# Performance work log

Measured on AMD Instinct MI355X. Metric: run time of the kernel, lower is better.

The kernel has to match this reference:

```python
import jax, jax.numpy as jnp
import numpy as np

N, E = 50000, 800000
IN, HID, OUT = 128, 256, 40
EPS = 1e-5


def setup_inputs() -> dict:
    key = jax.random.key(0)
    ks = jax.random.split(key, 16)
    def glorot(k, shape):
        lim = float(np.sqrt(6.0 / (shape[0] + shape[1])))
        return jax.random.uniform(k, shape, jnp.float32, -lim, lim)
    return {
        "x": jax.random.normal(ks[0], (N, IN), jnp.float32),
        "edge_index": jax.random.randint(ks[1], (2, E), 0, N, jnp.int64),
        "W1": glorot(ks[2], (IN, HID)),  "b1": jnp.zeros((HID,), jnp.float32),
        "g1": jnp.ones((HID,), jnp.float32), "be1": jnp.zeros((HID,), jnp.float32),
        "W2": glorot(ks[3], (HID, HID)), "b2": jnp.zeros((HID,), jnp.float32),
        "g2": jnp.ones((HID,), jnp.float32), "be2": jnp.zeros((HID,), jnp.float32),
        "W3": glorot(ks[4], (HID, OUT)), "b3": jnp.zeros((OUT,), jnp.float32),
        "Wl": glorot(ks[5], (OUT, OUT)), "bl": jnp.zeros((OUT,), jnp.float32),
    }


def _gcn_conv(h, src, dst, norm, W, b, n):
    # PyG GCNConv: transform, then normalized scatter-add over edges (+self-loops)
    m = h @ W                                     # [N, d_out]
    msg = m[src] * norm[:, None]                  # gather + edge scale
    out = jax.ops.segment_sum(msg, dst, num_segments=n)
    return out + b


def _bn(h, g, b):
    # BatchNorm1d (training-mode batch stats, biased variance)
    mu = jnp.mean(h, axis=0)
    var = jnp.var(h, axis=0)
    return (h - mu) * jax.lax.rsqrt(var + EPS) * g + b


def reference(x, edge_index, W1, b1, g1, be1, W2, b2, g2, be2, W3, b3, Wl, bl):
    n = x.shape[0]
    loops = jnp.arange(n, dtype=edge_index.dtype)
    src = jnp.concatenate([edge_index[0], loops])
    dst = jnp.concatenate([edge_index[1], loops])
    deg = jax.ops.segment_sum(jnp.ones(src.shape[0], x.dtype), dst, num_segments=n)
    dinv = jnp.where(deg > 0, jax.lax.rsqrt(deg), 0.0)
    norm = dinv[src] * dinv[dst]

    h = jax.nn.relu(_bn(_gcn_conv(x, src, dst, norm, W1, b1, n), g1, be1))
    h = jax.nn.relu(_bn(_gcn_conv(h, src, dst, norm, W2, b2, n), g2, be2))
    h = _gcn_conv(h, src, dst, norm, W3, b3, n)
    h = h @ Wl + bl
    return jax.nn.log_softmax(h, axis=1)
```

## Files before the change

kernel.cpp:

```cpp
#include <hip/hip_runtime.h>
#include <hip/hip_bf16.h>
#include <math.h>

#define IN_DIM 128
#define HID 256
#define OUT_DIM 40
#define OUT_PAD 64
#define CAP 64
#define EPS 1e-5f

typedef __attribute__((ext_vector_type(8))) short short8;
typedef __attribute__((ext_vector_type(4))) float floatx4;

__device__ __forceinline__ float b2f(unsigned short u) {
    union { unsigned int i; float f; } c; c.i = ((unsigned int)u) << 16; return c.f;
}
__device__ __forceinline__ unsigned short f2b(float f) {
    union { float f; unsigned int i; } c; c.f = f;
    unsigned int r = c.i + 0x7FFF + ((c.i >> 16) & 1);
    return (unsigned short)(r >> 16);
}

union U8 { uint4 u; unsigned short s[8]; };
union F8 { short8 v; unsigned short s[8]; uint4 u; };


__global__ void fill1_k(const int* __restrict__ src, const int* __restrict__ dst,
                        int* __restrict__ cnt, int* __restrict__ col2, int E,
                        const float* __restrict__ W1, const float* __restrict__ W2,
                        const float* __restrict__ W3, const float* __restrict__ Wl,
                        const float* __restrict__ b3, const float* __restrict__ bl,
                        unsigned short* __restrict__ W1t, unsigned short* __restrict__ W2t,
                        unsigned short* __restrict__ W3lt, float* __restrict__ bias2,
                        float* __restrict__ stats1, float* __restrict__ stats2,
                        const float* __restrict__ x, unsigned short* __restrict__ xb,
                        int N) {
    if (blockIdx.x < 1024) {
        for (int e = blockIdx.x * 256 + threadIdx.x; e < E; e += 1024 * 256) {
            int d = dst[e];
            int p = atomicAdd(&cnt[d], 1);
            if (p < CAP) col2[d * CAP + p] = src[e];
        }
    } else if (blockIdx.x < 1536) {
        const int n1 = 256 * 128, n2 = 256 * 256;
        int j = (blockIdx.x - 1024) * 256 + threadIdx.x;
        if (j < n1) {
            int n = j >> 7, k = j & 127;
            W1t[j] = f2b(W1[k * 256 + n]);
        } else if (j < n1 + n2) {
            int j2 = j - n1;
            int n = j2 >> 8, k = j2 & 255;
            W2t[j2] = f2b(W2[k * 256 + n]);
        } else {
            int j3 = j - n1 - n2;
            int n = j3 >> 8, k = j3 & 255;
            float acc = 0.f;
            if (n < OUT_DIM) {
                for (int q = 0; q < OUT_DIM; ++q)
                    acc += W3[k * OUT_DIM + q] * Wl[q * OUT_DIM + n];
            }
            W3lt[j3] = (n < OUT_DIM) ? f2b(acc) : 0;
            if (j3 < OUT_DIM) {
                float b = bl[j3];
                for (int q = 0; q < OUT_DIM; ++q) b += b3[q] * Wl[q * OUT_DIM + j3];
                bias2[j3] = b;
            }
        }
    } else if (blockIdx.x == 1536) {
        int t = threadIdx.x;
        stats1[t] = 0.f; stats1[256 + t] = 0.f;
        stats2[t] = 0.f; stats2[256 + t] = 0.f;
    } else {
        size_t nx = (size_t)N * 32;
        size_t nbk = gridDim.x - 1537;
        for (size_t i = (size_t)(blockIdx.x - 1537) * 256 + threadIdx.x; i < nx;
             i += nbk * 256) {
            float4 v = ((const float4*)x)[i];
            ushort4 o;
            o.x = f2b(v.x); o.y = f2b(v.y); o.z = f2b(v.z); o.w = f2b(v.w);
            ((ushort4*)xb)[i] = o;
        }
    }
}


template <int MT, bool BN, bool STATS>
__global__ __launch_bounds__(64, 6) void gemm_w(const unsigned short* __restrict__ A,
                                                const unsigned short* __restrict__ Bt,
                                                unsigned short* __restrict__ C,
                                                const int* __restrict__ cnt,
                                                const float* __restrict__ bias,
                                                const float* __restrict__ bnstats,
                                                const float* __restrict__ g,
                                                const float* __restrict__ be,
                                                float* __restrict__ gstats,
                                                float invN,
                                                int M, int Nc, int K, int ldc) {
    __shared__ float s_sc[BN ? HID : 1], s_sh[BN ? HID : 1];
    int lane = threadIdx.x;
    if (BN) {
        for (int t = lane; t < K; t += 64) {
            float mu = bnstats[t] * invN;
            float var = bnstats[HID + t] * invN - mu * mu;
            float sc = g[t] * rsqrtf(var + EPS);
            s_sc[t] = sc;
            s_sh[t] = be[t] - mu * sc;
        }
        __syncthreads();
    }
    int r16 = lane & 15, quad = lane >> 4;
    int row0 = blockIdx.y * (MT * 16), col0 = blockIdx.x * 64;

    int arow[MT];
#pragma unroll
    for (int mt = 0; mt < MT; ++mt) arow[mt] = min(row0 + mt * 16 + r16, M - 1);

    floatx4 acc[MT][4] = {};

    for (int k0 = 0; k0 < K; k0 += 32) {
        int ka = k0 + quad * 8;
        F8 a[MT], b[4];
#pragma unroll
        for (int mt = 0; mt < MT; ++mt)
            a[mt].u = *(const uint4*)&A[(size_t)arow[mt] * K + ka];
#pragma unroll
        for (int nt = 0; nt < 4; ++nt)
            b[nt].u = *(const uint4*)&Bt[(size_t)(col0 + nt * 16 + r16) * K + ka];
        if (BN) {
            float4 sc0 = *(const float4*)&s_sc[ka];
            float4 sc1 = *(const float4*)&s_sc[ka + 4];
            float4 sh0 = *(const float4*)&s_sh[ka];
            float4 sh1 = *(const float4*)&s_sh[ka + 4];
            float sc[8] = {sc0.x, sc0.y, sc0.z, sc0.w, sc1.x, sc1.y, sc1.z, sc1.w};
            float sh[8] = {sh0.x, sh0.y, sh0.z, sh0.w, sh1.x, sh1.y, sh1.z, sh1.w};
#pragma unroll
            for (int mt = 0; mt < MT; ++mt)
#pragma unroll
                for (int j = 0; j < 8; ++j) {
                    float f = b2f(a[mt].s[j]) * sc[j] + sh[j];
                    a[mt].s[j] = f2b(fmaxf(f, 0.f));
                }
        }
#pragma unroll
        for (int mt = 0; mt < MT; ++mt)
#pragma unroll
            for (int nt = 0; nt < 4; ++nt)
                acc[mt][nt] = __builtin_amdgcn_mfma_f32_16x16x32_bf16(a[mt].v, b[nt].v, acc[mt][nt], 0, 0, 0);
    }

    float s1[4] = {0.f, 0.f, 0.f, 0.f}, s2[4] = {0.f, 0.f, 0.f, 0.f};
#pragma unroll
    for (int mt = 0; mt < MT; ++mt) {
#pragma unroll
        for (int r = 0; r < 4; ++r) {
            int row = row0 + mt * 16 + quad * 4 + r;
            if (row >= M) continue;
            float dv = cnt ? rsqrtf((float)(cnt[row] + 1)) : 1.f;
#pragma unroll
            for (int nt = 0; nt < 4; ++nt) {
                int colg = col0 + nt * 16 + r16;
                if (colg < Nc) {
                    float v = acc[mt][nt][r] * dv + (bias ? bias[colg] : 0.f);
                    C[(size_t)row * ldc + colg] = f2b(v);
                    if (STATS) { s1[nt] += v; s2[nt] += v * v; }
                }
            }
        }
    }
    if (STATS) {
#pragma unroll
        for (int nt = 0; nt < 4; ++nt) {
            s1[nt] += __shfl_xor(s1[nt], 16); s1[nt] += __shfl_xor(s1[nt], 32);
            s2[nt] += __shfl_xor(s2[nt], 16); s2[nt] += __shfl_xor(s2[nt], 32);
            if (quad == 0) {
                int colg = col0 + nt * 16 + r16;
                atomicAdd(&gstats[colg], s1[nt]);
                atomicAdd(&gstats[HID + colg], s2[nt]);
            }
        }
    }
}


__global__ __launch_bounds__(256, 8) void agg_x(const unsigned short* __restrict__ m,
                                                const int* __restrict__ col2,
                                                const int* __restrict__ cnt,
                                                unsigned short* __restrict__ out,
                                                int N) {
    int v = blockIdx.x * 4 + (threadIdx.x >> 6);
    if (v >= N) return;
    int lane = threadIdx.x & 63;
    int q = lane >> 4;
    int c0 = (lane & 15) * 8;
    int cv = cnt[v];
    float dv = rsqrtf((float)(cv + 1));
    const int* col = col2 + v * CAP;
    int end = min(cv, CAP);
    float a[8] = {};
    {
        U8 r; r.u = *(const uint4*)&m[(size_t)v * IN_DIM + c0];
#pragma unroll
        for (int k = 0; k < 8; ++k) a[k] = b2f(r.s[k]) * dv;
    }
    if (q != 0) { a[0]=a[1]=a[2]=a[3]=a[4]=a[5]=a[6]=a[7]=0.f; }
    int e = 0;
    for (; e + 8 <= end; e += 8) {
        int idx[2];
#pragma unroll
        for (int j = 0; j < 2; ++j) idx[j] = col[e + 4 * j + q];
        float ds[2];
#pragma unroll
        for (int j = 0; j < 2; ++j) ds[j] = rsqrtf((float)(cnt[idx[j]] + 1));
        U8 rr[2];
#pragma unroll
        for (int j = 0; j < 2; ++j)
            rr[j].u = *(const uint4*)&m[(size_t)idx[j] * IN_DIM + c0];
#pragma unroll
        for (int j = 0; j < 2; ++j)
#pragma unroll
            for (int k = 0; k < 8; ++k) a[k] += b2f(rr[j].s[k]) * ds[j];
    }
    for (; e < end; e += 4) {
        int t = e + q;
        if (t < end) {
            int s = col[t];
            float ds = rsqrtf((float)(cnt[s] + 1));
            U8 r; r.u = *(const uint4*)&m[(size_t)s * IN_DIM + c0];
#pragma unroll
            for (int k = 0; k < 8; ++k) a[k] += b2f(r.s[k]) * ds;
        }
    }
#pragma unroll
    for (int k = 0; k < 8; ++k) {
        a[k] += __shfl_xor(a[k], 16);
        a[k] += __shfl_xor(a[k], 32);
    }
    if (q == 0) {
        U8 o;
#pragma unroll
        for (int k = 0; k < 8; ++k) o.s[k] = f2b(a[k] * dv);
        *(uint4*)&out[(size_t)v * IN_DIM + c0] = o.u;
    }
}

__global__ __launch_bounds__(256, 8) void agg_h(const unsigned short* __restrict__ m,
                                                const int* __restrict__ col2,
                                                const int* __restrict__ cnt,
                                                const float* __restrict__ bias,
                                                unsigned short* __restrict__ out,
                                                int N) {
    int v = blockIdx.x * 4 + (threadIdx.x >> 6);
    if (v >= N) return;
    int lane = threadIdx.x & 63;
    int half = lane >> 5;
    int c0 = (lane & 31) * 8;
    int cv = cnt[v];
    float dv = rsqrtf((float)(cv + 1));
    const int* col = col2 + v * CAP;
    int end = min(cv, CAP);
    float a[8] = {};
    if (half == 0) {
        U8 r; r.u = *(const uint4*)&m[(size_t)v * HID + c0];
#pragma unroll
        for (int k = 0; k < 8; ++k) a[k] = b2f(r.s[k]);
    }
    int e = 0;
    for (; e + 8 <= end; e += 8) {
        int idx[4];
#pragma unroll
        for (int j = 0; j < 4; ++j) idx[j] = col[e + 2 * j + half];
        U8 rr[4];
#pragma unroll
        for (int j = 0; j < 4; ++j)
            rr[j].u = *(const uint4*)&m[(size_t)idx[j] * HID + c0];
#pragma unroll
        for (int j = 0; j < 4; ++j)
#pragma unroll
            for (int k = 0; k < 8; ++k) a[k] += b2f(rr[j].s[k]);
    }
    for (; e < end; e += 2) {
        int t = e + half;
        if (t < end) {
            U8 r; r.u = *(const uint4*)&m[(size_t)col[t] * HID + c0];
#pragma unroll
            for (int k = 0; k < 8; ++k) a[k] += b2f(r.s[k]);
        }
    }
#pragma unroll
    for (int k = 0; k < 8; ++k) a[k] += __shfl_xor(a[k], 32);
    if (half == 0) {
        U8 o;
#pragma unroll
        for (int k = 0; k < 8; ++k) o.s[k] = f2b(a[k] * dv + bias[c0 + k]);
        *(uint4*)&out[(size_t)v * HID + c0] = o.u;
    }
}

__global__ __launch_bounds__(256, 8) void agg_o_ls(const unsigned short* __restrict__ m,
                                                   const int* __restrict__ col2,
                                                   const int* __restrict__ cnt,
                                                   const float* __restrict__ bias2,
                                                   float* __restrict__ out,
                                                   int N) {
    int v = blockIdx.x * 4 + (threadIdx.x >> 6);
    if (v >= N) return;
    int lane = threadIdx.x & 63;
    int slot = lane >> 3;
    int li = lane & 7;
    int c0 = li * 8;
    int cv = cnt[v];
    float dv = rsqrtf((float)(cv + 1));
    const int* col = col2 + v * CAP;
    int end = min(cv, CAP);
    float a[8] = {};
    if (slot == 0) {
        U8 r; r.u = *(const uint4*)&m[(size_t)v * OUT_PAD + c0];
#pragma unroll
        for (int k = 0; k < 8; ++k) a[k] = b2f(r.s[k]);
    }
    int e = 0;
    for (; e + 16 <= end; e += 16) {
        int idx[2];
        idx[0] = col[e + slot];
        idx[1] = col[e + 8 + slot];
        U8 rr[2];
#pragma unroll
        for (int j = 0; j < 2; ++j)
            rr[j].u = *(const uint4*)&m[(size_t)idx[j] * OUT_PAD + c0];
#pragma unroll
        for (int j = 0; j < 2; ++j)
#pragma unroll
            for (int k = 0; k < 8; ++k) a[k] += b2f(rr[j].s[k]);
    }
    for (; e < end; e += 8) {
        int t = e + slot;
        if (t < end) {
            U8 r; r.u = *(const uint4*)&m[(size_t)col[t] * OUT_PAD + c0];
#pragma unroll
            for (int k = 0; k < 8; ++k) a[k] += b2f(r.s[k]);
        }
    }
#pragma unroll
    for (int k = 0; k < 8; ++k) {
        a[k] += __shfl_xor(a[k], 8);
        a[k] += __shfl_xor(a[k], 16);
        a[k] += __shfl_xor(a[k], 32);
    }
    bool valid = (li < 5);
    float mx = -INFINITY;
#pragma unroll
    for (int k = 0; k < 8; ++k) {
        float val = valid ? (a[k] * dv + bias2[c0 + k]) : -INFINITY;
        a[k] = val;
        mx = fmaxf(mx, val);
    }
    mx = fmaxf(mx, __shfl_xor(mx, 1));
    mx = fmaxf(mx, __shfl_xor(mx, 2));
    mx = fmaxf(mx, __shfl_xor(mx, 4));
    float s = 0.f;
    if (valid) {
#pragma unroll
        for (int k = 0; k < 8; ++k) s += expf(a[k] - mx);
    }
    s += __shfl_xor(s, 1);
    s += __shfl_xor(s, 2);
    s += __shfl_xor(s, 4);
    float ls = mx + logf(s);
    if (slot == 0 && valid) {
        float4 o0, o1;
        o0.x = a[0] - ls; o0.y = a[1] - ls; o0.z = a[2] - ls; o0.w = a[3] - ls;
        o1.x = a[4] - ls; o1.y = a[5] - ls; o1.z = a[6] - ls; o1.w = a[7] - ls;
        float* p = &out[(size_t)v * OUT_DIM + c0];
        *(float4*)p = o0;
        *(float4*)(p + 4) = o1;
    }
}


__global__ __launch_bounds__(256) void bn_stats(const unsigned short* __restrict__ h,
                                                float* __restrict__ stats, int N) {
    __shared__ float ls[8][2][256];
    int t = threadIdx.x;
    int walker = t >> 5;
    int c0 = (t & 31) * 8;
    int r0 = blockIdx.x * 128;
    int rend = min(r0 + 128, N);
    float s1[8] = {}, s2[8] = {};
    for (int r = r0 + walker; r < rend; r += 8) {
        U8 x; x.u = *(const uint4*)&h[(size_t)r * HID + c0];
#pragma unroll
        for (int k = 0; k < 8; ++k) {
            float v = b2f(x.s[k]);
            s1[k] += v; s2[k] += v * v;
        }
    }
#pragma unroll
    for (int k = 0; k < 8; ++k) {
        ls[walker][0][c0 + k] = s1[k];
        ls[walker][1][c0 + k] = s2[k];
    }
    __syncthreads();
    float a1 = 0.f, a2 = 0.f;
#pragma unroll
    for (int w = 0; w < 8; ++w) { a1 += ls[w][0][t]; a2 += ls[w][1][t]; }
    atomicAdd(&stats[t], a1);
    atomicAdd(&stats[HID + t], a2);
}


extern "C" void kernel_launch(void* const* d_in, const int* in_sizes, int n_in,
                              void* d_out, int out_size, void* d_ws, size_t ws_size,
                              hipStream_t stream) {
    const float* x   = (const float*)d_in[0];
    const int*  eidx = (const int*)d_in[1];
    const float* W1 = (const float*)d_in[2];
    const float* b1 = (const float*)d_in[3];
    const float* g1 = (const float*)d_in[4];
    const float* be1 = (const float*)d_in[5];
    const float* W2 = (const float*)d_in[6];
    const float* b2 = (const float*)d_in[7];
    const float* g2 = (const float*)d_in[8];
    const float* be2 = (const float*)d_in[9];
    const float* W3 = (const float*)d_in[10];
    const float* b3 = (const float*)d_in[11];
    const float* Wl = (const float*)d_in[12];
    const float* bl = (const float*)d_in[13];
    float* out = (float*)d_out;

    const int N = in_sizes[0] / IN_DIM;
    const int E = in_sizes[1] / 2;
    const int* src = eidx;
    const int* dst = eidx + E;

    size_t off = 0;
    char* ws = (char*)d_ws;
    auto carve = [&](size_t bytes) -> void* {
        void* p = ws + off;
        off += (bytes + 255) & ~(size_t)255;
        return p;
    };
    int*   cnt  = (int*)carve((size_t)N * 4);
    float* stats1 = (float*)carve((size_t)2 * HID * 4);
    float* stats2 = (float*)carve((size_t)2 * HID * 4);
    int*   col2 = (int*)carve((size_t)N * CAP * 4);
    unsigned short* xb   = (unsigned short*)carve((size_t)N * IN_DIM * 2);
    unsigned short* axb  = (unsigned short*)carve((size_t)N * IN_DIM * 2);
    unsigned short* W1t  = (unsigned short*)carve((size_t)256 * IN_DIM * 2);
    unsigned short* W2t  = (unsigned short*)carve((size_t)256 * HID * 2);
    unsigned short* W3lt = (unsigned short*)carve((size_t)128 * HID * 2);
    float* bias2 = (float*)carve((size_t)OUT_DIM * 4);
    unsigned short* mbuf = (unsigned short*)carve((size_t)N * HID * 2);
    unsigned short* hbuf = (unsigned short*)carve((size_t)N * HID * 2);

    hipMemsetAsync(cnt, 0, (size_t)N * 4, stream);
    int xconvBlocks = (int)(((size_t)N * 32 + 255) / 256);
    fill1_k<<<1537 + xconvBlocks, 256, 0, stream>>>(src, dst, cnt, col2, E,
                                                    W1, W2, W3, Wl, b3, bl,
                                                    W1t, W2t, W3lt, bias2,
                                                    stats1, stats2, x, xb, N);

    int nodeBlocks = (N + 3) / 4;
    float invN = 1.f / (float)N;
    int mb32 = (N + 31) / 32;
    int mb16 = (N + 15) / 16;

    agg_x<<<nodeBlocks, 256, 0, stream>>>(xb, col2, cnt, axb, N);
    gemm_w<2, false, true><<<dim3(4, mb32), 64, 0, stream>>>(axb, W1t, hbuf,
                                                             nullptr, b1,
                                                             nullptr, nullptr, nullptr,
                                                             stats1, invN,
                                                             N, HID, IN_DIM, HID);

    gemm_w<2, true, false><<<dim3(4, mb32), 64, 0, stream>>>(hbuf, W2t, mbuf,
                                                             cnt, nullptr,
                                                             stats1, g1, be1,
                                                             nullptr, invN,
                                                             N, HID, HID, HID);
    agg_h<<<nodeBlocks, 256, 0, stream>>>(mbuf, col2, cnt, b2, hbuf, N);
    bn_stats<<<(N + 127) / 128, 256, 0, stream>>>(hbuf, stats2, N);

    gemm_w<1, true, false><<<dim3(1, mb16), 64, 0, stream>>>(hbuf, W3lt, mbuf,
                                                             cnt, nullptr,
                                                             stats2, g2, be2,
                                                             nullptr, invN,
                                                             N, OUT_PAD, HID, OUT_PAD);
    agg_o_ls<<<nodeBlocks, 256, 0, stream>>>(mbuf, col2, cnt, bias2, out, N);
}
```

Baseline: 422.8 us.

## Stage GEMM tiles in LDS across multi-wave blocks and shrink CSR indices to 16-bit

Replaces the single-wave register-direct GEMM with a multi-wave kernel that stages A and B tiles through shared memory, so the B (weight) tile is loaded once per block and shared by 2-4 waves. BN stats are reduced in shared memory before the global atomics. The neighbor index buffer is stored as unsigned short, halving its footprint and gather traffic. The edge-fill phase also gets twice as many blocks. The 16-bit indices only hold for N ≤ 65536, so correctness depends on the input size. The new GEMM adds two block barriers per K step.

```diff
diff --git a/kernel.cpp b/kernel.cpp
--- a/kernel.cpp
+++ b/kernel.cpp
@@ -26,7 +26,7 @@
 
 
 __global__ void fill1_k(const int* __restrict__ src, const int* __restrict__ dst,
-                        int* __restrict__ cnt, int* __restrict__ col2, int E,
+                        int* __restrict__ cnt, unsigned short* __restrict__ col2, int E,
                         const float* __restrict__ W1, const float* __restrict__ W2,
                         const float* __restrict__ W3, const float* __restrict__ Wl,
                         const float* __restrict__ b3, const float* __restrict__ bl,
@@ -35,15 +35,15 @@
                         float* __restrict__ stats1, float* __restrict__ stats2,
                         const float* __restrict__ x, unsigned short* __restrict__ xb,
                         int N) {
-    if (blockIdx.x < 1024) {
-        for (int e = blockIdx.x * 256 + threadIdx.x; e < E; e += 1024 * 256) {
+    if (blockIdx.x < 2048) {
+        for (int e = blockIdx.x * 256 + threadIdx.x; e < E; e += 2048 * 256) {
             int d = dst[e];
             int p = atomicAdd(&cnt[d], 1);
-            if (p < CAP) col2[d * CAP + p] = src[e];
-        }
-    } else if (blockIdx.x < 1536) {
+            if (p < CAP) col2[(size_t)d * CAP + p] = (unsigned short)src[e];
+        }
+    } else if (blockIdx.x < 2560) {
         const int n1 = 256 * 128, n2 = 256 * 256;
-        int j = (blockIdx.x - 1024) * 256 + threadIdx.x;
+        int j = (blockIdx.x - 2048) * 256 + threadIdx.x;
         if (j < n1) {
             int n = j >> 7, k = j & 127;
             W1t[j] = f2b(W1[k * 256 + n]);
@@ -66,14 +66,14 @@
                 bias2[j3] = b;
             }
         }
-    } else if (blockIdx.x == 1536) {
+    } else if (blockIdx.x == 2560) {
         int t = threadIdx.x;
         stats1[t] = 0.f; stats1[256 + t] = 0.f;
         stats2[t] = 0.f; stats2[256 + t] = 0.f;
     } else {
         size_t nx = (size_t)N * 32;
-        size_t nbk = gridDim.x - 1537;
-        for (size_t i = (size_t)(blockIdx.x - 1537) * 256 + threadIdx.x; i < nx;
+        size_t nbk = gridDim.x - 2561;
+        for (size_t i = (size_t)(blockIdx.x - 2561) * 256 + threadIdx.x; i < nx;
              i += nbk * 256) {
             float4 v = ((const float4*)x)[i];
             ushort4 o;
@@ -84,86 +84,88 @@
 }
 
 
-template <int MT, bool BN, bool STATS>
-__global__ __launch_bounds__(64, 6) void gemm_w(const unsigned short* __restrict__ A,
-                                                const unsigned short* __restrict__ Bt,
-                                                unsigned short* __restrict__ C,
-                                                const int* __restrict__ cnt,
-                                                const float* __restrict__ bias,
-                                                const float* __restrict__ bnstats,
-                                                const float* __restrict__ g,
-                                                const float* __restrict__ be,
-                                                float* __restrict__ gstats,
-                                                float invN,
-                                                int M, int Nc, int K, int ldc) {
+template <int NW, bool BN, bool STATS>
+__global__ __launch_bounds__(NW * 64) void gemm_t(const unsigned short* __restrict__ A,
+                                                  const unsigned short* __restrict__ Bt,
+                                                  unsigned short* __restrict__ C,
+                                                  const int* __restrict__ cnt,
+                                                  const float* __restrict__ bias,
+                                                  const float* __restrict__ bnstats,
+                                                  const float* __restrict__ g,
+                                                  const float* __restrict__ be,
+                                                  float* __restrict__ gstats,
+                                                  float invN,
+                                                  int M, int Nc, int K, int ldc) {
+    __shared__ unsigned short As[NW * 16][40];
+    __shared__ unsigned short Bs[64][40];
     __shared__ float s_sc[BN ? HID : 1], s_sh[BN ? HID : 1];
-    int lane = threadIdx.x;
+    __shared__ float ls1[STATS ? 64 : 1], ls2[STATS ? 64 : 1];
+    int tid = threadIdx.x;
     if (BN) {
-        for (int t = lane; t < K; t += 64) {
+        for (int t = tid; t < K; t += NW * 64) {
             float mu = bnstats[t] * invN;
             float var = bnstats[HID + t] * invN - mu * mu;
             float sc = g[t] * rsqrtf(var + EPS);
             s_sc[t] = sc;
             s_sh[t] = be[t] - mu * sc;
         }
+    }
+    if (STATS && tid < 64) { ls1[tid] = 0.f; ls2[tid] = 0.f; }
+    __syncthreads();
+
+    int wave = tid >> 6, lane = tid & 63;
+    int r16 = lane & 15, quad = lane >> 4;
+    int row0 = blockIdx.y * (NW * 16), col0 = blockIdx.x * 64;
+
+    floatx4 acc[4] = {};
+
+    int sr = tid >> 2, sko = (tid & 3) * 8;
+    for (int k0 = 0; k0 < K; k0 += 32) {
+        {
+            int ar = min(row0 + sr, M - 1);
+            U8 ra;
+            ra.u = *(const uint4*)&A[(size_t)ar * K + k0 + sko];
+            if (BN) {
+#pragma unroll
+                for (int j = 0; j < 8; ++j) {
+                    int kk = k0 + sko + j;
+                    float f = b2f(ra.s[j]) * s_sc[kk] + s_sh[kk];
+                    ra.s[j] = f2b(fmaxf(f, 0.f));
+                }
+            }
+            *(uint4*)&As[sr][sko] = ra.u;
+        }
+#pragma unroll
+        for (int j = 0; j < 4 / NW; ++j) {
+            int idx = tid + j * NW * 64;
+            int br = idx >> 2, bko = (idx & 3) * 8;
+            *(uint4*)&Bs[br][bko] = *(const uint4*)&Bt[(size_t)(col0 + br) * K + k0 + bko];
+        }
         __syncthreads();
-    }
-    int r16 = lane & 15, quad = lane >> 4;
-    int row0 = blockIdx.y * (MT * 16), col0 = blockIdx.x * 64;
-
-    int arow[MT];
-#pragma unroll
-    for (int mt = 0; mt < MT; ++mt) arow[mt] = min(row0 + mt * 16 + r16, M - 1);
-
-    floatx4 acc[MT][4] = {};
-
-    for (int k0 = 0; k0 < K; k0 += 32) {
-        int ka = k0 + quad * 8;
-        F8 a[MT], b[4];
-#pragma unroll
-        for (int mt = 0; mt < MT; ++mt)
-            a[mt].u = *(const uint4*)&A[(size_t)arow[mt] * K + ka];
+        F8 a, b[4];
+        a.u = *(const uint4*)&As[wave * 16 + r16][quad * 8];
 #pragma unroll
         for (int nt = 0; nt < 4; ++nt)
-            b[nt].u = *(const uint4*)&Bt[(size_t)(col0 + nt * 16 + r16) * K + ka];
-        if (BN) {
-            float4 sc0 = *(const float4*)&s_sc[ka];
-            float4 sc1 = *(const float4*)&s_sc[ka + 4];
-            float4 sh0 = *(const float4*)&s_sh[ka];
-            float4 sh1 = *(const float4*)&s_sh[ka + 4];
-            float sc[8] = {sc0.x, sc0.y, sc0.z, sc0.w, sc1.x, sc1.y, sc1.z, sc1.w};
-            float sh[8] = {sh0.x, sh0.y, sh0.z, sh0.w, sh1.x, sh1.y, sh1.z, sh1.w};
-#pragma unroll
-            for (int mt = 0; mt < MT; ++mt)
-#pragma unroll
-                for (int j = 0; j < 8; ++j) {
-                    float f = b2f(a[mt].s[j]) * sc[j] + sh[j];
-                    a[mt].s[j] = f2b(fmaxf(f, 0.f));
-                }
-        }
-#pragma unroll
-        for (int mt = 0; mt < MT; ++mt)
-#pragma unroll
-            for (int nt = 0; nt < 4; ++nt)
-                acc[mt][nt] = __builtin_amdgcn_mfma_f32_16x16x32_bf16(a[mt].v, b[nt].v, acc[mt][nt], 0, 0, 0);
+            b[nt].u = *(const uint4*)&Bs[nt * 16 + r16][quad * 8];
+#pragma unroll
+        for (int nt = 0; nt < 4; ++nt)
+            acc[nt] = __builtin_amdgcn_mfma_f32_16x16x32_bf16(a.v, b[nt].v, acc[nt], 0, 0, 0);
+        __syncthreads();
     }
 
     float s1[4] = {0.f, 0.f, 0.f, 0.f}, s2[4] = {0.f, 0.f, 0.f, 0.f};
 #pragma unroll
-    for (int mt = 0; mt < MT; ++mt) {
-#pragma unroll
-        for (int r = 0; r < 4; ++r) {
-            int row = row0 + mt * 16 + quad * 4 + r;
-            if (row >= M) continue;
-            float dv = cnt ? rsqrtf((float)(cnt[row] + 1)) : 1.f;
-#pragma unroll
-            for (int nt = 0; nt < 4; ++nt) {
-                int colg = col0 + nt * 16 + r16;
-                if (colg < Nc) {
-                    float v = acc[mt][nt][r] * dv + (bias ? bias[colg] : 0.f);
-                    C[(size_t)row * ldc + colg] = f2b(v);
-                    if (STATS) { s1[nt] += v; s2[nt] += v * v; }
-                }
+    for (int r = 0; r < 4; ++r) {
+        int row = row0 + wave * 16 + quad * 4 + r;
+        if (row >= M) continue;
+        float dv = cnt ? rsqrtf((float)(cnt[row] + 1)) : 1.f;
+#pragma unroll
+        for (int nt = 0; nt < 4; ++nt) {
+            int colg = col0 + nt * 16 + r16;
+            if (colg < Nc) {
+                float v = acc[nt][r] * dv + (bias ? bias[colg] : 0.f);
+                C[(size_t)row * ldc + colg] = f2b(v);
+                if (STATS) { s1[nt] += v; s2[nt] += v * v; }
             }
         }
     }
@@ -173,17 +175,22 @@
             s1[nt] += __shfl_xor(s1[nt], 16); s1[nt] += __shfl_xor(s1[nt], 32);
             s2[nt] += __shfl_xor(s2[nt], 16); s2[nt] += __shfl_xor(s2[nt], 32);
             if (quad == 0) {
-                int colg = col0 + nt * 16 + r16;
-                atomicAdd(&gstats[colg], s1[nt]);
-                atomicAdd(&gstats[HID + colg], s2[nt]);
+                atomicAdd(&ls1[nt * 16 + r16], s1[nt]);
+                atomicAdd(&ls2[nt * 16 + r16], s2[nt]);
             }
         }
+        __syncthreads();
+        if (tid < 64) {
+            int cg = col0 + tid;
+            atomicAdd(&gstats[cg], ls1[tid]);
+            atomicAdd(&gstats[HID + cg], ls2[tid]);
+        }
     }
 }
 
 
 __global__ __launch_bounds__(256, 8) void agg_x(const unsigned short* __restrict__ m,
-                                                const int* __restrict__ col2,
+                                                const unsigned short* __restrict__ col2,
                                                 const int* __restrict__ cnt,
                                                 unsigned short* __restrict__ out,
                                                 int N) {
@@ -194,7 +201,7 @@
     int c0 = (lane & 15) * 8;
     int cv = cnt[v];
     float dv = rsqrtf((float)(cv + 1));
-    const int* col = col2 + v * CAP;
+    const unsigned short* col = col2 + (size_t)v * CAP;
     int end = min(cv, CAP);
     float a[8] = {};
     {
@@ -244,7 +251,7 @@
 }
 
 __global__ __launch_bounds__(256, 8) void agg_h(const unsigned short* __restrict__ m,
-                                                const int* __restrict__ col2,
+                                                const unsigned short* __restrict__ col2,
                                                 const int* __restrict__ cnt,
                                                 const float* __restrict__ bias,
                                                 unsigned short* __restrict__ out,
@@ -256,7 +263,7 @@
     int c0 = (lane & 31) * 8;
     int cv = cnt[v];
     float dv = rsqrtf((float)(cv + 1));
-    const int* col = col2 + v * CAP;
+    const unsigned short* col = col2 + (size_t)v * CAP;
     int end = min(cv, CAP);
     float a[8] = {};
     if (half == 0) {
@@ -297,7 +304,7 @@
 }
 
 __global__ __launch_bounds__(256, 8) void agg_o_ls(const unsigned short* __restrict__ m,
-                                                   const int* __restrict__ col2,
+                                                   const unsigned short* __restrict__ col2,
                                                    const int* __restrict__ cnt,
                                                    const float* __restrict__ bias2,
                                                    float* __restrict__ out,
@@ -310,7 +317,7 @@
     int c0 = li * 8;
     int cv = cnt[v];
     float dv = rsqrtf((float)(cv + 1));
-    const int* col = col2 + v * CAP;
+    const unsigned short* col = col2 + (size_t)v * CAP;
     int end = min(cv, CAP);
     float a[8] = {};
     if (slot == 0) {
@@ -442,7 +449,7 @@
     int*   cnt  = (int*)carve((size_t)N * 4);
     float* stats1 = (float*)carve((size_t)2 * HID * 4);
     float* stats2 = (float*)carve((size_t)2 * HID * 4);
-    int*   col2 = (int*)carve((size_t)N * CAP * 4);
+    unsigned short* col2 = (unsigned short*)carve((size_t)N * CAP * 2);
     unsigned short* xb   = (unsigned short*)carve((size_t)N * IN_DIM * 2);
     unsigned short* axb  = (unsigned short*)carve((size_t)N * IN_DIM * 2);
     unsigned short* W1t  = (unsigned short*)carve((size_t)256 * IN_DIM * 2);
@@ -454,35 +461,35 @@
 
     hipMemsetAsync(cnt, 0, (size_t)N * 4, stream);
     int xconvBlocks = (int)(((size_t)N * 32 + 255) / 256);
-    fill1_k<<<1537 + xconvBlocks, 256, 0, stream>>>(src, dst, cnt, col2, E,
+    fill1_k<<<2561 + xconvBlocks, 256, 0, stream>>>(src, dst, cnt, col2, E,
                                                     W1, W2, W3, Wl, b3, bl,
                                                     W1t, W2t, W3lt, bias2,
                                                     stats1, stats2, x, xb, N);
 
     int nodeBlocks = (N + 3) / 4;
     float invN = 1.f / (float)N;
+    int mb64 = (N + 63) / 64;
     int mb32 = (N + 31) / 32;
-    int mb16 = (N + 15) / 16;
 
     agg_x<<<nodeBlocks, 256, 0, stream>>>(xb, col2, cnt, axb, N);
-    gemm_w<2, false, true><<<dim3(4, mb32), 64, 0, stream>>>(axb, W1t, hbuf,
-                                                             nullptr, b1,
-                                                             nullptr, nullptr, nullptr,
-                                                             stats1, invN,
-                                                             N, HID, IN_DIM, HID);
-
-    gemm_w<2, true, false><<<dim3(4, mb32), 64, 0, stream>>>(hbuf, W2t, mbuf,
-                                                             cnt, nullptr,
-                                                             stats1, g1, be1,
-                                                             nullptr, invN,
-                                                             N, HID, HID, HID);
+    gemm_t<4, false, true><<<dim3(4, mb64), 256, 0, stream>>>(axb, W1t, hbuf,
+                                                              nullptr, b1,
+                                                              nullptr, nullptr, nullptr,
+                                                              stats1, invN,
+                                                              N, HID, IN_DIM, HID);
+
+    gemm_t<4, true, false><<<dim3(4, mb64), 256, 0, stream>>>(hbuf, W2t, mbuf,
+                                                              cnt, nullptr,
+                                                              stats1, g1, be1,
+                                                              nullptr, invN,
+                                                              N, HID, HID, HID);
     agg_h<<<nodeBlocks, 256, 0, stream>>>(mbuf, col2, cnt, b2, hbuf, N);
     bn_stats<<<(N + 127) / 128, 256, 0, stream>>>(hbuf, stats2, N);
 
-    gemm_w<1, true, false><<<dim3(1, mb16), 64, 0, stream>>>(hbuf, W3lt, mbuf,
-                                                             cnt, nullptr,
-                                                             stats2, g2, be2,
-                                                             nullptr, invN,
-                                                             N, OUT_PAD, HID, OUT_PAD);
+    gemm_t<2, true, false><<<dim3(1, mb32), 128, 0, stream>>>(hbuf, W3lt, mbuf,
+                                                              cnt, nullptr,
+                                                              stats2, g2, be2,
+                                                              nullptr, invN,
+                                                              N, OUT_PAD, HID, OUT_PAD);
     agg_o_ls<<<nodeBlocks, 256, 0, stream>>>(mbuf, col2, cnt, bias2, out, N);
 }
```

Result: faster. 366.2 us (-13.4%).
